# Performance work log

Hardware: AMD Instinct MI355X
Metric: run time of the kernel (lower is better)

## Reference

```python
import jax, jax.numpy as jnp
import numpy as np

L = 8      # subsequence_len
A = 4      # alphabet_size
D = 256    # sketch_dim
SEQ = 16384


def setup_inputs() -> dict:
    key = jax.random.key(0)
    k1, k2, k3 = jax.random.split(key, 3)
    sequence = jax.random.randint(k1, (SEQ,), 0, A)
    # stacked nn.Embedding weights: (L, A, D), init N(0, 0.5)
    hash_emb = 0.5 * jax.random.normal(k2, (L, A, D), dtype=jnp.float32)
    sign_logits = 0.5 * jax.random.normal(k3, (L, A), dtype=jnp.float32)
    return {"sequence": sequence, "hash_emb": hash_emb, "sign_logits": sign_logits}


def _forward(sequence, hash_emb, sign_logits):
    # roll_idx[j, s] = (j - s) % D  so that gather reproduces torch.roll(t, s)[j] = t[(j - s) % D]
    roll_idx = (jnp.arange(D)[:, None] - jnp.arange(D)[None, :]) % D
    p_arr = jnp.arange(1, L + 1, dtype=jnp.float32)           # p = 1..L
    Tp0 = jnp.zeros((L + 1, D), dtype=jnp.float32).at[0, 0].set(1.0)
    Tm0 = jnp.zeros((L + 1, D), dtype=jnp.float32)

    def step(carry, xs):
        Tp, Tm = carry                                         # (L+1, D) each
        c, i = xs
        valid = (c >= 0) & (c < A)
        c_safe = jnp.clip(c, 0, A - 1)
        # eval-mode soft hash: softmax over the embedding row (per level p)
        probs = jax.nn.softmax(hash_emb[:, c_safe, :], axis=-1)   # (L, D)
        sign = jax.nn.sigmoid(sign_logits[:, c_safe])             # (L,)
        denom = (i + 1).astype(jnp.float32)
        # z = p/(i+1); levels with p > i+1 (and invalid chars) are frozen (z=0)
        z = jnp.where((p_arr <= denom) & valid, p_arr / denom, 0.0)  # (L,)
        Tp_prev, Tm_prev = Tp[:L], Tm[:L]                         # (L, D)
        # expected circular shift: out[l, j] = sum_s probs[l, s] * T_prev[l, (j-s)%D]
        stp = jnp.einsum('ljs,ls->lj', Tp_prev[:, roll_idx], probs)
        stm = jnp.einsum('ljs,ls->lj', Tm_prev[:, roll_idx], probs)
        s = sign[:, None]
        upd_p = s * stp + (1.0 - s) * stm
        upd_m = s * stm + (1.0 - s) * stp
        zc = z[:, None]
        new_Tp = Tp.at[1:].set((1.0 - zc) * Tp[1:] + zc * upd_p)
        new_Tm = Tm.at[1:].set((1.0 - zc) * Tm[1:] + zc * upd_m)
        return (new_Tp, new_Tm), None

    step = jax.checkpoint(step)
    (Tp, Tm), _ = jax.lax.scan(step, (Tp0, Tm0), (sequence, jnp.arange(SEQ)))
    return Tp[L] - Tm[L]


def reference(sequence, hash_emb, sign_logits):
    return _forward(sequence, hash_emb, sign_logits)
```

## Files before the change

kernel.cpp:

```cpp
#include <hip/hip_runtime.h>
#include <math.h>

#define LL 8
#define AA 4
#define DD 256
#define KF 129
#define KH 128
#define CLEN 64
#define NES 36
#define LPAD 37

typedef float v2f __attribute__((ext_vector_type(2)));

#define SIX(l2,l1) ((((l2)*((l2)-1))>>1) + (l1))
#define SLOT(s)    ((s)*LPAD + ((s)>>1))

#define V_OFF   0
#define CNT_OFF (2 * KF)

__device__ __forceinline__ float invCN8() {
  constexpr double c = (16384.0 * 16383.0 * 16382.0 * 16381.0 *
                        16380.0 * 16379.0 * 16378.0 * 16377.0) / 40320.0;
  return (float)(1.0 / c);
}

__device__ __forceinline__ v2f cfma(const v2f b, const v2f a, v2f acc) {
  const v2f bb = (v2f){ b.x,  b.x};
  const v2f bw = (v2f){-b.y,  b.y};
  const v2f as = (v2f){ a.y,  a.x};
  acc = __builtin_elementwise_fma(bb, a,  acc);
  acc = __builtin_elementwise_fma(bw, as, acc);
  return acc;
}

template <unsigned MASK>
__device__ __forceinline__ void prodCols(const v2f* __restrict__ A, const v2f* __restrict__ B,
                                         v2f (&o)[NES]) {
#pragma unroll
  for (int l1 = 0; l1 < 8; ++l1) {
    if ((MASK >> l1) & 1) {
#pragma unroll
      for (int l2 = l1 + 1; l2 <= 8; ++l2) {
        v2f acc = A[SIX(l2, l1)] + B[SIX(l2, l1)];
#pragma unroll
        for (int m = l1 + 1; m < l2; ++m) acc = cfma(B[SIX(l2, m)], A[SIX(m, l1)], acc);
        o[SIX(l2, l1)] = acc;
      }
    }
  }
}

template <unsigned MASK>
__device__ __forceinline__ void writeCols(v2f* __restrict__ D, const v2f (&o)[NES]) {
#pragma unroll
  for (int l1 = 0; l1 < 8; ++l1) {
    if ((MASK >> l1) & 1) {
#pragma unroll
      for (int l2 = l1 + 1; l2 <= 8; ++l2) D[SIX(l2, l1)] = o[SIX(l2, l1)];
    }
  }
}

__device__ __forceinline__ void prodFullRA(const v2f (&A)[NES], const v2f* __restrict__ B,
                                           v2f (&o)[NES]) {
#pragma unroll
  for (int l1 = 0; l1 < 8; ++l1) {
#pragma unroll
    for (int l2 = l1 + 1; l2 <= 8; ++l2) {
      v2f acc = A[SIX(l2, l1)] + B[SIX(l2, l1)];
#pragma unroll
      for (int m = l1 + 1; m < l2; ++m) acc = cfma(B[SIX(l2, m)], A[SIX(m, l1)], acc);
      o[SIX(l2, l1)] = acc;
    }
  }
}

__device__ __forceinline__ void prodR(const float* __restrict__ A, const float* __restrict__ B,
                                      float (&o)[NES]) {
#pragma unroll
  for (int l1 = 0; l1 < 8; ++l1) {
#pragma unroll
    for (int l2 = l1 + 1; l2 <= 8; ++l2) {
      float acc = A[SIX(l2, l1)] + B[SIX(l2, l1)];
#pragma unroll
      for (int m = l1 + 1; m < l2; ++m) acc = fmaf(B[SIX(l2, m)], A[SIX(m, l1)], acc);
      o[SIX(l2, l1)] = acc;
    }
  }
}

__global__ __launch_bounds__(256, 1) void kmain(const int* __restrict__ seq,
                                                const float* __restrict__ hemb,
                                                const float* __restrict__ slog,
                                                float* __restrict__ v,
                                                int* __restrict__ cnt,
                                                float* __restrict__ outp) {
  const int blk = blockIdx.x;
  const int t   = threadIdx.x;
  __shared__ __align__(16) float ldsf[9600];
  __shared__ __align__(16) float4 qtab[LL * AA];
  __shared__ float2 twd[256];
  __shared__ float dvr[KF], dvi[KF];
  __shared__ int isLast;

  {
    float sn, cs;
    __sincosf((float)t * 0.0245436926061702596754894014319f, &sn, &cs);
    twd[t] = make_float2(cs, sn);
  }
  __syncthreads();

  {
    const int r  = t >> 3;
    const int g8 = t & 7;
    float4 hv[8];
#pragma unroll
    for (int u = 0; u < 8; ++u)
      hv[u] = *(const float4*)(hemb + r * DD + u * 32 + g8 * 4);
    float mx = -1e30f;
#pragma unroll
    for (int u = 0; u < 8; ++u) {
      mx = fmaxf(mx, fmaxf(fmaxf(hv[u].x, hv[u].y), fmaxf(hv[u].z, hv[u].w)));
    }
    mx = fmaxf(mx, __shfl_xor(mx, 1));
    mx = fmaxf(mx, __shfl_xor(mx, 2));
    mx = fmaxf(mx, __shfl_xor(mx, 4));

    float sum = 0.0f, cr = 0.0f, ci = 0.0f;
    if (blk < KH) {
      const int k = blk;
#pragma unroll
      for (int u = 0; u < 8; ++u) {
        const float ev[4] = {expf(hv[u].x - mx), expf(hv[u].y - mx),
                             expf(hv[u].z - mx), expf(hv[u].w - mx)};
#pragma unroll
        for (int w = 0; w < 4; ++w) {
          const int j = u * 32 + g8 * 4 + w;
          const int m = (j * k) & 255;
          const float2 tv = twd[m];
          sum += ev[w];
          cr = fmaf(ev[w], tv.x, cr);
          ci = fmaf(-ev[w], tv.y, ci);
        }
      }
    } else {
#pragma unroll
      for (int u = 0; u < 8; ++u) {
        const float ev[4] = {expf(hv[u].x - mx), expf(hv[u].y - mx),
                             expf(hv[u].z - mx), expf(hv[u].w - mx)};
        sum += ev[0] + ev[1] + ev[2] + ev[3];
        cr  += (ev[0] - ev[1]) + (ev[2] - ev[3]);
      }
    }
    sum += __shfl_xor(sum, 1); cr += __shfl_xor(cr, 1); ci += __shfl_xor(ci, 1);
    sum += __shfl_xor(sum, 2); cr += __shfl_xor(cr, 2); ci += __shfl_xor(ci, 2);
    sum += __shfl_xor(sum, 4); cr += __shfl_xor(cr, 4); ci += __shfl_xor(ci, 4);

    if (g8 == 0) {
      const float sl = slog[r];
      const float sg = 1.0f / (1.0f + expf(-sl));
      const float q  = fmaf(2.0f, sg, -1.0f);
      const float sc = q / sum;
      const float qr = cr * sc;
      const float qi = ci * sc;
      qtab[r] = make_float4(qr, qr, -qi, qi);
    }
  }
  __syncthreads();

  if (blk < KH) {
    const int k = blk;

    v2f G[NES];
#pragma unroll
    for (int e = 0; e < NES; ++e) G[e] = (v2f){0.f, 0.f};

    const int4* sp = (const int4*)(seq + t * CLEN);
    for (int sb = 0; sb < CLEN / 4; ++sb) {
      const int4 cs = sp[sb];
      const int csy[4] = {cs.x, cs.y, cs.z, cs.w};
#pragma unroll
      for (int u = 0; u < 4; ++u) {
        const int c = csy[u];
        float4 qv[LL];
#pragma unroll
        for (int l = 0; l < LL; ++l) qv[l] = qtab[(l << 2) | c];
#pragma unroll
        for (int l = LL; l >= 1; --l) {
          const float4 q4 = qv[l - 1];
          const v2f qa = (v2f){q4.x, q4.y};
          const v2f qb = (v2f){q4.z, q4.w};
          {
            v2f g = G[SIX(l, l - 1)];
            g.x += q4.x; g.y += q4.w;
            G[SIX(l, l - 1)] = g;
          }
#pragma unroll
          for (int l1 = 0; l1 < l - 1; ++l1) {
            const v2f H  = G[SIX(l - 1, l1)];
            const v2f Hs = (v2f){H.y, H.x};
            v2f g = G[SIX(l, l1)];
            g = __builtin_elementwise_fma(qa, H,  g);
            g = __builtin_elementwise_fma(qb, Hs, g);
            G[SIX(l, l1)] = g;
          }
        }
      }
    }

    v2f* L = (v2f*)ldsf;
    if (t & 1) {
      v2f* D = L + SLOT(t >> 1);
#pragma unroll
      for (int e = 0; e < NES; ++e) D[e] = G[e];
    }
    __syncthreads();
    if (!(t & 1)) {
      v2f o[NES];
      prodFullRA(G, L + SLOT(t >> 1), o);
      v2f* D = L + SLOT(t >> 1);
#pragma unroll
      for (int e = 0; e < NES; ++e) D[e] = o[e];
    }
    __syncthreads();

    const int w = t >> 6;
    const int j = t & 63;
    v2f pc[NES];
    for (int n = 64; n >= 8; n >>= 1) {
      const bool act = (j < n);
      if (act) {
        const v2f* Ab = L + SLOT(2 * j);
        const v2f* Bb = L + SLOT(2 * j + 1);
        switch (w) {
          case 0:  prodCols<0x01>(Ab, Bb, pc); break;
          case 1:  prodCols<0x42>(Ab, Bb, pc); break;
          case 2:  prodCols<0x14>(Ab, Bb, pc); break;
          default: prodCols<0xA8>(Ab, Bb, pc); break;
        }
      }
      __syncthreads();
      if (act) {
        v2f* Db = L + SLOT(j);
        switch (w) {
          case 0:  writeCols<0x01>(Db, pc); break;
          case 1:  writeCols<0x42>(Db, pc); break;
          case 2:  writeCols<0x14>(Db, pc); break;
          default: writeCols<0xA8>(Db, pc); break;
        }
      }
      __syncthreads();
    }

    if (t < 64) {
      v2f sv[LL + 1];
      sv[0] = (v2f){1.f, 0.f};
#pragma unroll
      for (int l = 1; l <= LL; ++l) sv[l] = (v2f){0.f, 0.f};
      for (int gg = 0; gg < 8; ++gg) {
        v2f nv = (v2f){0.f, 0.f};
        if (t >= 1 && t <= LL) {
          nv = sv[t];
          const v2f* Bb = L + SLOT(gg);
          const int rb = (t * (t - 1)) >> 1;
#pragma unroll
          for (int l1 = 0; l1 < 8; ++l1) {
            if (l1 < t) nv = cfma(Bb[rb + l1], sv[l1], nv);
          }
        }
#pragma unroll
        for (int l = 1; l <= LL; ++l) {
          sv[l].x = __shfl(nv.x, l);
          sv[l].y = __shfl(nv.y, l);
        }
      }
      if (t == 0) {
        __hip_atomic_store(&v[2 * k],     sv[LL].x, __ATOMIC_RELEASE, __HIP_MEMORY_SCOPE_AGENT);
        __hip_atomic_store(&v[2 * k + 1], sv[LL].y, __ATOMIC_RELEASE, __HIP_MEMORY_SCOPE_AGENT);
      }
    }
  } else {
    float* Lr = ldsf;
    float Q8[LL][AA];
#pragma unroll
    for (int lc = 0; lc < LL * AA; ++lc) Q8[lc >> 2][lc & 3] = qtab[lc].x;

    float Gr[NES];
#pragma unroll
    for (int e = 0; e < NES; ++e) Gr[e] = 0.f;

    const int4* sp = (const int4*)(seq + t * CLEN);
    for (int sb = 0; sb < CLEN / 4; ++sb) {
      const int4 cs = sp[sb];
      const int csy[4] = {cs.x, cs.y, cs.z, cs.w};
#pragma unroll
      for (int u = 0; u < 4; ++u) {
        const int c = csy[u];
        float Qs[LL];
#pragma unroll
        for (int l = 0; l < LL; ++l) {
          const float qa = (c & 1) ? Q8[l][1] : Q8[l][0];
          const float qb = (c & 1) ? Q8[l][3] : Q8[l][2];
          Qs[l] = (c & 2) ? qb : qa;
        }
#pragma unroll
        for (int l = LL; l >= 1; --l) {
          Gr[SIX(l, l - 1)] += Qs[l - 1];
#pragma unroll
          for (int l1 = 0; l1 < l - 1; ++l1)
            Gr[SIX(l, l1)] = fmaf(Qs[l - 1], Gr[SIX(l - 1, l1)], Gr[SIX(l, l1)]);
        }
      }
    }
#pragma unroll
    for (int e = 0; e < NES; ++e) Lr[t * LPAD + e] = Gr[e];
    __syncthreads();

    float po[NES];
    for (int n = 128; n >= 1; n >>= 1) {
      const bool act = (t < n);
      if (act) prodR(Lr + (2 * t) * LPAD, Lr + (2 * t + 1) * LPAD, po);
      __syncthreads();
      if (act) { for (int e = 0; e < NES; ++e) Lr[t * LPAD + e] = po[e]; }
      __syncthreads();
    }
    if (t == 0) {
      __hip_atomic_store(&v[2 * KH],     Lr[SIX(LL, 0)], __ATOMIC_RELEASE, __HIP_MEMORY_SCOPE_AGENT);
      __hip_atomic_store(&v[2 * KH + 1], 0.0f,           __ATOMIC_RELEASE, __HIP_MEMORY_SCOPE_AGENT);
    }
  }

  __syncthreads();
  if (t == 0) {
    const int old = __hip_atomic_fetch_add(&cnt[0], 1, __ATOMIC_ACQ_REL, __HIP_MEMORY_SCOPE_AGENT);
    isLast = (old == KH) ? 1 : 0;
  }
  __syncthreads();
  if (isLast) {
    if (t < KF) {
      dvr[t] = __hip_atomic_load(&v[2 * t],     __ATOMIC_ACQUIRE, __HIP_MEMORY_SCOPE_AGENT);
      dvi[t] = __hip_atomic_load(&v[2 * t + 1], __ATOMIC_ACQUIRE, __HIP_MEMORY_SCOPE_AGENT);
    }
    if (t == 0) {
      __hip_atomic_store(&cnt[0], 0, __ATOMIC_RELEASE, __HIP_MEMORY_SCOPE_AGENT);
    }
    __syncthreads();
    const float sc = (1.0f / 256.0f) * invCN8();
    float sum = dvr[0] + ((t & 1) ? -dvr[KH] : dvr[KH]);
    for (int k2 = 1; k2 < KH; ++k2) {
      const int m = (t * k2) & 255;
      const float2 wv = twd[m];
      sum = fmaf(2.0f * dvr[k2], wv.x, sum);
      sum = fmaf(-2.0f * dvi[k2], wv.y, sum);
    }
    outp[t] = sum * sc;
  }
}

extern "C" void kernel_launch(void* const* d_in, const int* in_sizes, int n_in,
                              void* d_out, int out_size, void* d_ws, size_t ws_size,
                              hipStream_t stream) {
  (void)in_sizes; (void)n_in; (void)out_size; (void)ws_size;
  const int*   seq  = (const int*)d_in[0];
  const float* hemb = (const float*)d_in[1];
  const float* slog = (const float*)d_in[2];
  float* ws   = (float*)d_ws;
  float* v    = ws + V_OFF;
  int*   cnt  = (int*)(ws + CNT_OFF);
  float* o    = (float*)d_out;

  hipMemsetAsync(cnt, 0, sizeof(int), stream);
  hipLaunchKernelGGL(kmain, dim3(KF), dim3(256), 0, stream, seq, hemb, slog, v, cnt, o);
}
```

Before: 95.86 us.

## Split each frequency's sequence scan across four blocks and pair real frequencies

The grid grows from 129 blocks to 512. Each frequency is now handled by four blocks, each scanning a quarter of the sequence with 16-character chunks per thread. The two real frequencies (k=0 and k=128) are packed into one block using the two lanes of the v2f. Partial transfer operators are written to global memory, and the last block of each group of four combines them through per-frequency atomic counters. This gives more parallelism on a GPU with many compute units, in exchange for an extra cross-block reduction, more atomics and workspace traffic, and repeated setup work in every block.

```diff
diff --git a/kernel.cpp b/kernel.cpp
--- a/kernel.cpp
+++ b/kernel.cpp
@@ -6,7 +6,7 @@
 #define DD 256
 #define KF 129
 #define KH 128
-#define CLEN 64
+#define CLEN 16
 #define NES 36
 #define LPAD 37
 
@@ -16,7 +16,8 @@
 #define SLOT(s)    ((s)*LPAD + ((s)>>1))
 
 #define V_OFF   0
-#define CNT_OFF (2 * KF)
+#define VP_OFF  (2*KF)
+#define CNT_OFF (VP_OFF + 128*4*NES*2)
 
 __device__ __forceinline__ float invCN8() {
   constexpr double c = (16384.0 * 16383.0 * 16382.0 * 16381.0 *
@@ -24,16 +25,21 @@
   return (float)(1.0 / c);
 }
 
-__device__ __forceinline__ v2f cfma(const v2f b, const v2f a, v2f acc) {
-  const v2f bb = (v2f){ b.x,  b.x};
-  const v2f bw = (v2f){-b.y,  b.y};
-  const v2f as = (v2f){ a.y,  a.x};
-  acc = __builtin_elementwise_fma(bb, a,  acc);
-  acc = __builtin_elementwise_fma(bw, as, acc);
-  return acc;
-}
-
-template <unsigned MASK>
+template <bool R2>
+__device__ __forceinline__ v2f opfma(const v2f b, const v2f a, v2f acc) {
+  if (R2) {
+    return __builtin_elementwise_fma(b, a, acc);
+  } else {
+    const v2f bb = (v2f){ b.x,  b.x};
+    const v2f bw = (v2f){-b.y,  b.y};
+    const v2f as = (v2f){ a.y,  a.x};
+    acc = __builtin_elementwise_fma(bb, a,  acc);
+    acc = __builtin_elementwise_fma(bw, as, acc);
+    return acc;
+  }
+}
+
+template <unsigned MASK, bool R2>
 __device__ __forceinline__ void prodCols(const v2f* __restrict__ A, const v2f* __restrict__ B,
                                          v2f (&o)[NES]) {
 #pragma unroll
@@ -43,7 +49,7 @@
       for (int l2 = l1 + 1; l2 <= 8; ++l2) {
         v2f acc = A[SIX(l2, l1)] + B[SIX(l2, l1)];
 #pragma unroll
-        for (int m = l1 + 1; m < l2; ++m) acc = cfma(B[SIX(l2, m)], A[SIX(m, l1)], acc);
+        for (int m = l1 + 1; m < l2; ++m) acc = opfma<R2>(B[SIX(l2, m)], A[SIX(m, l1)], acc);
         o[SIX(l2, l1)] = acc;
       }
     }
@@ -61,6 +67,7 @@
   }
 }
 
+template <bool R2>
 __device__ __forceinline__ void prodFullRA(const v2f (&A)[NES], const v2f* __restrict__ B,
                                            v2f (&o)[NES]) {
 #pragma unroll
@@ -69,132 +76,54 @@
     for (int l2 = l1 + 1; l2 <= 8; ++l2) {
       v2f acc = A[SIX(l2, l1)] + B[SIX(l2, l1)];
 #pragma unroll
-      for (int m = l1 + 1; m < l2; ++m) acc = cfma(B[SIX(l2, m)], A[SIX(m, l1)], acc);
+      for (int m = l1 + 1; m < l2; ++m) acc = opfma<R2>(B[SIX(l2, m)], A[SIX(m, l1)], acc);
       o[SIX(l2, l1)] = acc;
     }
   }
 }
 
-__device__ __forceinline__ void prodR(const float* __restrict__ A, const float* __restrict__ B,
-                                      float (&o)[NES]) {
-#pragma unroll
-  for (int l1 = 0; l1 < 8; ++l1) {
-#pragma unroll
-    for (int l2 = l1 + 1; l2 <= 8; ++l2) {
-      float acc = A[SIX(l2, l1)] + B[SIX(l2, l1)];
-#pragma unroll
-      for (int m = l1 + 1; m < l2; ++m) acc = fmaf(B[SIX(l2, m)], A[SIX(m, l1)], acc);
-      o[SIX(l2, l1)] = acc;
-    }
-  }
-}
-
-__global__ __launch_bounds__(256, 1) void kmain(const int* __restrict__ seq,
-                                                const float* __restrict__ hemb,
-                                                const float* __restrict__ slog,
-                                                float* __restrict__ v,
-                                                int* __restrict__ cnt,
-                                                float* __restrict__ outp) {
-  const int blk = blockIdx.x;
-  const int t   = threadIdx.x;
-  __shared__ __align__(16) float ldsf[9600];
-  __shared__ __align__(16) float4 qtab[LL * AA];
-  __shared__ float2 twd[256];
-  __shared__ float dvr[KF], dvi[KF];
-  __shared__ int isLast;
-
-  {
-    float sn, cs;
-    __sincosf((float)t * 0.0245436926061702596754894014319f, &sn, &cs);
-    twd[t] = make_float2(cs, sn);
-  }
-  __syncthreads();
-
-  {
-    const int r  = t >> 3;
-    const int g8 = t & 7;
-    float4 hv[8];
-#pragma unroll
-    for (int u = 0; u < 8; ++u)
-      hv[u] = *(const float4*)(hemb + r * DD + u * 32 + g8 * 4);
-    float mx = -1e30f;
-#pragma unroll
-    for (int u = 0; u < 8; ++u) {
-      mx = fmaxf(mx, fmaxf(fmaxf(hv[u].x, hv[u].y), fmaxf(hv[u].z, hv[u].w)));
-    }
-    mx = fmaxf(mx, __shfl_xor(mx, 1));
-    mx = fmaxf(mx, __shfl_xor(mx, 2));
-    mx = fmaxf(mx, __shfl_xor(mx, 4));
-
-    float sum = 0.0f, cr = 0.0f, ci = 0.0f;
-    if (blk < KH) {
-      const int k = blk;
-#pragma unroll
-      for (int u = 0; u < 8; ++u) {
-        const float ev[4] = {expf(hv[u].x - mx), expf(hv[u].y - mx),
-                             expf(hv[u].z - mx), expf(hv[u].w - mx)};
-#pragma unroll
-        for (int w = 0; w < 4; ++w) {
-          const int j = u * 32 + g8 * 4 + w;
-          const int m = (j * k) & 255;
-          const float2 tv = twd[m];
-          sum += ev[w];
-          cr = fmaf(ev[w], tv.x, cr);
-          ci = fmaf(-ev[w], tv.y, ci);
-        }
-      }
-    } else {
-#pragma unroll
-      for (int u = 0; u < 8; ++u) {
-        const float ev[4] = {expf(hv[u].x - mx), expf(hv[u].y - mx),
-                             expf(hv[u].z - mx), expf(hv[u].w - mx)};
-        sum += ev[0] + ev[1] + ev[2] + ev[3];
-        cr  += (ev[0] - ev[1]) + (ev[2] - ev[3]);
-      }
-    }
-    sum += __shfl_xor(sum, 1); cr += __shfl_xor(cr, 1); ci += __shfl_xor(ci, 1);
-    sum += __shfl_xor(sum, 2); cr += __shfl_xor(cr, 2); ci += __shfl_xor(ci, 2);
-    sum += __shfl_xor(sum, 4); cr += __shfl_xor(cr, 4); ci += __shfl_xor(ci, 4);
-
-    if (g8 == 0) {
-      const float sl = slog[r];
-      const float sg = 1.0f / (1.0f + expf(-sl));
-      const float q  = fmaf(2.0f, sg, -1.0f);
-      const float sc = q / sum;
-      const float qr = cr * sc;
-      const float qi = ci * sc;
-      qtab[r] = make_float4(qr, qr, -qi, qi);
-    }
-  }
-  __syncthreads();
-
-  if (blk < KH) {
-    const int k = blk;
-
-    v2f G[NES];
-#pragma unroll
-    for (int e = 0; e < NES; ++e) G[e] = (v2f){0.f, 0.f};
-
-    const int4* sp = (const int4*)(seq + t * CLEN);
-    for (int sb = 0; sb < CLEN / 4; ++sb) {
-      const int4 cs = sp[sb];
-      const int csy[4] = {cs.x, cs.y, cs.z, cs.w};
-#pragma unroll
-      for (int u = 0; u < 4; ++u) {
-        const int c = csy[u];
-        float4 qv[LL];
-#pragma unroll
-        for (int l = 0; l < LL; ++l) qv[l] = qtab[(l << 2) | c];
-#pragma unroll
-        for (int l = LL; l >= 1; --l) {
-          const float4 q4 = qv[l - 1];
+template <bool R2>
+__device__ __forceinline__ void applyOp(v2f (&s)[LL + 1], const v2f* __restrict__ op) {
+#pragma unroll
+  for (int l2 = LL; l2 >= 1; --l2) {
+    v2f acc = s[l2];
+#pragma unroll
+    for (int m = 0; m < l2; ++m) acc = opfma<R2>(op[SIX(l2, m)], s[m], acc);
+    s[l2] = acc;
+  }
+}
+
+template <bool R2>
+__device__ __forceinline__ void bodyMain(const int* __restrict__ seq, v2f* L,
+                                         const float4* qtab, int t, int qtr) {
+  v2f G[NES];
+#pragma unroll
+  for (int e = 0; e < NES; ++e) G[e] = (v2f){0.f, 0.f};
+
+  const int ch = qtr * 256 + t;
+  const int4* sp = (const int4*)(seq + ch * CLEN);
+  for (int sb = 0; sb < CLEN / 4; ++sb) {
+    const int4 cs = sp[sb];
+    const int csy[4] = {cs.x, cs.y, cs.z, cs.w};
+#pragma unroll
+    for (int u = 0; u < 4; ++u) {
+      const int c = csy[u];
+      float4 qv[LL];
+#pragma unroll
+      for (int l = 0; l < LL; ++l) qv[l] = qtab[(l << 2) | c];
+#pragma unroll
+      for (int l = LL; l >= 1; --l) {
+        const float4 q4 = qv[l - 1];
+        if (R2) {
+          const v2f qa = (v2f){q4.x, q4.y};
+          G[SIX(l, l - 1)] += qa;
+#pragma unroll
+          for (int l1 = 0; l1 < l - 1; ++l1)
+            G[SIX(l, l1)] = __builtin_elementwise_fma(qa, G[SIX(l - 1, l1)], G[SIX(l, l1)]);
+        } else {
           const v2f qa = (v2f){q4.x, q4.y};
           const v2f qb = (v2f){q4.z, q4.w};
-          {
-            v2f g = G[SIX(l, l - 1)];
-            g.x += q4.x; g.y += q4.w;
-            G[SIX(l, l - 1)] = g;
-          }
+          { v2f g = G[SIX(l, l - 1)]; g.x += q4.x; g.y += q4.w; G[SIX(l, l - 1)] = g; }
 #pragma unroll
           for (int l1 = 0; l1 < l - 1; ++l1) {
             const v2f H  = G[SIX(l - 1, l1)];
@@ -207,133 +136,185 @@
         }
       }
     }
-
-    v2f* L = (v2f*)ldsf;
-    if (t & 1) {
-      v2f* D = L + SLOT(t >> 1);
-#pragma unroll
-      for (int e = 0; e < NES; ++e) D[e] = G[e];
+  }
+
+  if (t & 1) {
+    v2f* D = L + SLOT(t >> 1);
+#pragma unroll
+    for (int e = 0; e < NES; ++e) D[e] = G[e];
+  }
+  __syncthreads();
+  if (!(t & 1)) {
+    v2f o[NES];
+    prodFullRA<R2>(G, L + SLOT(t >> 1), o);
+    v2f* D = L + SLOT(t >> 1);
+#pragma unroll
+    for (int e = 0; e < NES; ++e) D[e] = o[e];
+  }
+  __syncthreads();
+
+  const int w = t >> 6;
+  const int j = t & 63;
+  v2f pc[NES];
+  for (int n = 64; n >= 1; n >>= 1) {
+    const bool act = (j < n);
+    if (act) {
+      const v2f* Ab = L + SLOT(2 * j);
+      const v2f* Bb = L + SLOT(2 * j + 1);
+      switch (w) {
+        case 0:  prodCols<0x01, R2>(Ab, Bb, pc); break;
+        case 1:  prodCols<0x42, R2>(Ab, Bb, pc); break;
+        case 2:  prodCols<0x14, R2>(Ab, Bb, pc); break;
+        default: prodCols<0xA8, R2>(Ab, Bb, pc); break;
+      }
     }
     __syncthreads();
-    if (!(t & 1)) {
-      v2f o[NES];
-      prodFullRA(G, L + SLOT(t >> 1), o);
-      v2f* D = L + SLOT(t >> 1);
-#pragma unroll
-      for (int e = 0; e < NES; ++e) D[e] = o[e];
+    if (act) {
+      v2f* Db = L + SLOT(j);
+      switch (w) {
+        case 0:  writeCols<0x01>(Db, pc); break;
+        case 1:  writeCols<0x42>(Db, pc); break;
+        case 2:  writeCols<0x14>(Db, pc); break;
+        default: writeCols<0xA8>(Db, pc); break;
+      }
     }
     __syncthreads();
-
-    const int w = t >> 6;
-    const int j = t & 63;
-    v2f pc[NES];
-    for (int n = 64; n >= 8; n >>= 1) {
-      const bool act = (j < n);
-      if (act) {
-        const v2f* Ab = L + SLOT(2 * j);
-        const v2f* Bb = L + SLOT(2 * j + 1);
-        switch (w) {
-          case 0:  prodCols<0x01>(Ab, Bb, pc); break;
-          case 1:  prodCols<0x42>(Ab, Bb, pc); break;
-          case 2:  prodCols<0x14>(Ab, Bb, pc); break;
-          default: prodCols<0xA8>(Ab, Bb, pc); break;
+  }
+}
+
+__global__ __launch_bounds__(256) void kmain(const int* __restrict__ seq,
+                                             const float* __restrict__ hemb,
+                                             const float* __restrict__ slog,
+                                             float* __restrict__ v,
+                                             float* __restrict__ vpart,
+                                             int* __restrict__ cnt,
+                                             float* __restrict__ outp) {
+  const int blk = blockIdx.x;
+  const int k   = blk >> 2;
+  const int qtr = blk & 3;
+  const int t   = threadIdx.x;
+  __shared__ __align__(16) float ldsf[9600];
+  __shared__ __align__(16) float4 qtab[LL * AA];
+  __shared__ float2 twd[256];
+  __shared__ float dvr[KF], dvi[KF];
+  __shared__ int isLast, isPairLast;
+
+  {
+    float sn, cs;
+    __sincosf((float)t * 0.0245436926061702596754894014319f, &sn, &cs);
+    twd[t] = make_float2(cs, sn);
+  }
+  __syncthreads();
+
+  {
+    const int r  = t >> 3;
+    const int g8 = t & 7;
+    float4 hv[8];
+#pragma unroll
+    for (int u = 0; u < 8; ++u)
+      hv[u] = *(const float4*)(hemb + r * DD + u * 32 + g8 * 4);
+    float mx = -1e30f;
+#pragma unroll
+    for (int u = 0; u < 8; ++u)
+      mx = fmaxf(mx, fmaxf(fmaxf(hv[u].x, hv[u].y), fmaxf(hv[u].z, hv[u].w)));
+    mx = fmaxf(mx, __shfl_xor(mx, 1));
+    mx = fmaxf(mx, __shfl_xor(mx, 2));
+    mx = fmaxf(mx, __shfl_xor(mx, 4));
+
+    float sum = 0.f, cr = 0.f, ci = 0.f;
+    if (k > 0) {
+#pragma unroll
+      for (int u = 0; u < 8; ++u) {
+        const float ev[4] = {expf(hv[u].x - mx), expf(hv[u].y - mx),
+                             expf(hv[u].z - mx), expf(hv[u].w - mx)};
+#pragma unroll
+        for (int w2 = 0; w2 < 4; ++w2) {
+          const int jj = u * 32 + g8 * 4 + w2;
+          const int m = (jj * k) & 255;
+          const float2 tv = twd[m];
+          sum += ev[w2];
+          cr = fmaf(ev[w2], tv.x, cr);
+          ci = fmaf(-ev[w2], tv.y, ci);
         }
       }
-      __syncthreads();
-      if (act) {
-        v2f* Db = L + SLOT(j);
-        switch (w) {
-          case 0:  writeCols<0x01>(Db, pc); break;
-          case 1:  writeCols<0x42>(Db, pc); break;
-          case 2:  writeCols<0x14>(Db, pc); break;
-          default: writeCols<0xA8>(Db, pc); break;
-        }
-      }
-      __syncthreads();
-    }
-
-    if (t < 64) {
-      v2f sv[LL + 1];
-      sv[0] = (v2f){1.f, 0.f};
-#pragma unroll
-      for (int l = 1; l <= LL; ++l) sv[l] = (v2f){0.f, 0.f};
-      for (int gg = 0; gg < 8; ++gg) {
-        v2f nv = (v2f){0.f, 0.f};
-        if (t >= 1 && t <= LL) {
-          nv = sv[t];
-          const v2f* Bb = L + SLOT(gg);
-          const int rb = (t * (t - 1)) >> 1;
-#pragma unroll
-          for (int l1 = 0; l1 < 8; ++l1) {
-            if (l1 < t) nv = cfma(Bb[rb + l1], sv[l1], nv);
-          }
-        }
-#pragma unroll
-        for (int l = 1; l <= LL; ++l) {
-          sv[l].x = __shfl(nv.x, l);
-          sv[l].y = __shfl(nv.y, l);
-        }
-      }
-      if (t == 0) {
-        __hip_atomic_store(&v[2 * k],     sv[LL].x, __ATOMIC_RELEASE, __HIP_MEMORY_SCOPE_AGENT);
-        __hip_atomic_store(&v[2 * k + 1], sv[LL].y, __ATOMIC_RELEASE, __HIP_MEMORY_SCOPE_AGENT);
-      }
-    }
-  } else {
-    float* Lr = ldsf;
-    float Q8[LL][AA];
-#pragma unroll
-    for (int lc = 0; lc < LL * AA; ++lc) Q8[lc >> 2][lc & 3] = qtab[lc].x;
-
-    float Gr[NES];
-#pragma unroll
-    for (int e = 0; e < NES; ++e) Gr[e] = 0.f;
-
-    const int4* sp = (const int4*)(seq + t * CLEN);
-    for (int sb = 0; sb < CLEN / 4; ++sb) {
-      const int4 cs = sp[sb];
-      const int csy[4] = {cs.x, cs.y, cs.z, cs.w};
-#pragma unroll
-      for (int u = 0; u < 4; ++u) {
-        const int c = csy[u];
-        float Qs[LL];
-#pragma unroll
-        for (int l = 0; l < LL; ++l) {
-          const float qa = (c & 1) ? Q8[l][1] : Q8[l][0];
-          const float qb = (c & 1) ? Q8[l][3] : Q8[l][2];
-          Qs[l] = (c & 2) ? qb : qa;
-        }
-#pragma unroll
-        for (int l = LL; l >= 1; --l) {
-          Gr[SIX(l, l - 1)] += Qs[l - 1];
-#pragma unroll
-          for (int l1 = 0; l1 < l - 1; ++l1)
-            Gr[SIX(l, l1)] = fmaf(Qs[l - 1], Gr[SIX(l - 1, l1)], Gr[SIX(l, l1)]);
-        }
-      }
-    }
-#pragma unroll
-    for (int e = 0; e < NES; ++e) Lr[t * LPAD + e] = Gr[e];
+    } else {
+#pragma unroll
+      for (int u = 0; u < 8; ++u) {
+        const float ev[4] = {expf(hv[u].x - mx), expf(hv[u].y - mx),
+                             expf(hv[u].z - mx), expf(hv[u].w - mx)};
+        sum += ev[0] + ev[1] + ev[2] + ev[3];
+        cr  += (ev[0] - ev[1]) + (ev[2] - ev[3]);
+      }
+    }
+    sum += __shfl_xor(sum, 1); cr += __shfl_xor(cr, 1); ci += __shfl_xor(ci, 1);
+    sum += __shfl_xor(sum, 2); cr += __shfl_xor(cr, 2); ci += __shfl_xor(ci, 2);
+    sum += __shfl_xor(sum, 4); cr += __shfl_xor(cr, 4); ci += __shfl_xor(ci, 4);
+
+    if (g8 == 0) {
+      const float sl = slog[r];
+      const float sg = 1.0f / (1.0f + expf(-sl));
+      const float q  = fmaf(2.0f, sg, -1.0f);
+      if (k > 0) {
+        const float qr = cr * q / sum;
+        const float qi = ci * q / sum;
+        qtab[r] = make_float4(qr, qr, -qi, qi);
+      } else {
+        qtab[r] = make_float4(q, cr * q / sum, 0.f, 0.f);
+      }
+    }
+  }
+  __syncthreads();
+
+  v2f* L = (v2f*)ldsf;
+  if (k == 0) bodyMain<true>(seq, L, qtab, t, qtr);
+  else        bodyMain<false>(seq, L, qtab, t, qtr);
+
+  if (t < NES) {
+    union { v2f v2; double d; } u;
+    u.v2 = L[t];
+    __hip_atomic_store((double*)vpart + (size_t)(k * 4 + qtr) * NES + t, u.d,
+                       __ATOMIC_RELEASE, __HIP_MEMORY_SCOPE_AGENT);
+  }
+  __syncthreads();
+  if (t == 0) {
+    const int old = __hip_atomic_fetch_add(&cnt[1 + k], 1, __ATOMIC_ACQ_REL, __HIP_MEMORY_SCOPE_AGENT);
+    isPairLast = (old == 3) ? 1 : 0;
+  }
+  __syncthreads();
+  if (isPairLast) {
+    if (t < 4 * NES) {
+      union { v2f v2; double d; } u;
+      u.d = __hip_atomic_load((const double*)vpart + (size_t)(k * 4) * NES + t,
+                              __ATOMIC_ACQUIRE, __HIP_MEMORY_SCOPE_AGENT);
+      L[t] = u.v2;
+    }
     __syncthreads();
-
-    float po[NES];
-    for (int n = 128; n >= 1; n >>= 1) {
-      const bool act = (t < n);
-      if (act) prodR(Lr + (2 * t) * LPAD, Lr + (2 * t + 1) * LPAD, po);
-      __syncthreads();
-      if (act) { for (int e = 0; e < NES; ++e) Lr[t * LPAD + e] = po[e]; }
-      __syncthreads();
-    }
     if (t == 0) {
-      __hip_atomic_store(&v[2 * KH],     Lr[SIX(LL, 0)], __ATOMIC_RELEASE, __HIP_MEMORY_SCOPE_AGENT);
-      __hip_atomic_store(&v[2 * KH + 1], 0.0f,           __ATOMIC_RELEASE, __HIP_MEMORY_SCOPE_AGENT);
+      v2f s[LL + 1];
+      s[0] = (k == 0) ? (v2f){1.f, 1.f} : (v2f){1.f, 0.f};
+#pragma unroll
+      for (int l = 1; l <= LL; ++l) s[l] = (v2f){0.f, 0.f};
+      for (int qq = 0; qq < 4; ++qq) {
+        const v2f* op = L + qq * NES;
+        if (k == 0) applyOp<true>(s, op); else applyOp<false>(s, op);
+      }
+      if (k == 0) {
+        __hip_atomic_store(&v[0],          s[LL].x, __ATOMIC_RELEASE, __HIP_MEMORY_SCOPE_AGENT);
+        __hip_atomic_store(&v[1],          0.0f,    __ATOMIC_RELEASE, __HIP_MEMORY_SCOPE_AGENT);
+        __hip_atomic_store(&v[2 * KH],     s[LL].y, __ATOMIC_RELEASE, __HIP_MEMORY_SCOPE_AGENT);
+        __hip_atomic_store(&v[2 * KH + 1], 0.0f,    __ATOMIC_RELEASE, __HIP_MEMORY_SCOPE_AGENT);
+      } else {
+        __hip_atomic_store(&v[2 * k],     s[LL].x, __ATOMIC_RELEASE, __HIP_MEMORY_SCOPE_AGENT);
+        __hip_atomic_store(&v[2 * k + 1], s[LL].y, __ATOMIC_RELEASE, __HIP_MEMORY_SCOPE_AGENT);
+      }
+      __hip_atomic_store(&cnt[1 + k], 0, __ATOMIC_RELAXED, __HIP_MEMORY_SCOPE_AGENT);
     }
   }
 
   __syncthreads();
   if (t == 0) {
     const int old = __hip_atomic_fetch_add(&cnt[0], 1, __ATOMIC_ACQ_REL, __HIP_MEMORY_SCOPE_AGENT);
-    isLast = (old == KH) ? 1 : 0;
+    isLast = (old == 511) ? 1 : 0;
   }
   __syncthreads();
   if (isLast) {
@@ -341,9 +322,8 @@
       dvr[t] = __hip_atomic_load(&v[2 * t],     __ATOMIC_ACQUIRE, __HIP_MEMORY_SCOPE_AGENT);
       dvi[t] = __hip_atomic_load(&v[2 * t + 1], __ATOMIC_ACQUIRE, __HIP_MEMORY_SCOPE_AGENT);
     }
-    if (t == 0) {
+    if (t == 0)
       __hip_atomic_store(&cnt[0], 0, __ATOMIC_RELEASE, __HIP_MEMORY_SCOPE_AGENT);
-    }
     __syncthreads();
     const float sc = (1.0f / 256.0f) * invCN8();
     float sum = dvr[0] + ((t & 1) ? -dvr[KH] : dvr[KH]);
@@ -364,11 +344,12 @@
   const int*   seq  = (const int*)d_in[0];
   const float* hemb = (const float*)d_in[1];
   const float* slog = (const float*)d_in[2];
-  float* ws   = (float*)d_ws;
-  float* v    = ws + V_OFF;
-  int*   cnt  = (int*)(ws + CNT_OFF);
-  float* o    = (float*)d_out;
-
-  hipMemsetAsync(cnt, 0, sizeof(int), stream);
-  hipLaunchKernelGGL(kmain, dim3(KF), dim3(256), 0, stream, seq, hemb, slog, v, cnt, o);
-}
+  float* ws    = (float*)d_ws;
+  float* v     = ws + V_OFF;
+  float* vpart = ws + VP_OFF;
+  int*   cnt   = (int*)(ws + CNT_OFF);
+  float* o     = (float*)d_out;
+
+  hipMemsetAsync(cnt, 0, (1 + KH) * sizeof(int), stream);
+  hipLaunchKernelGGL(kmain, dim3(512), dim3(256), 0, stream, seq, hemb, slog, v, vpart, cnt, o);
+}
```

Result: slower. 114.3 us (+19.3%).

## Double threads per block and halve per-thread chunk length

Applied to the files above, without the earlier changes.

Raises the block size from 256 to 512 threads and halves the sequence chunk each thread scans, so each thread does half the serial recurrence work. The softmax/DFT setup, the tree reductions and the LDS buffer are resized to match, which adds one more reduction level and doubles shared memory. The risk is higher register pressure at 512 threads per block and more synchronisation steps in the reduction.

```diff
diff --git a/kernel.cpp b/kernel.cpp
--- a/kernel.cpp
+++ b/kernel.cpp
@@ -6,7 +6,8 @@
 #define DD 256
 #define KF 129
 #define KH 128
-#define CLEN 64
+#define THR 512
+#define CLEN 32
 #define NES 36
 #define LPAD 37
 
@@ -89,7 +90,7 @@
   }
 }
 
-__global__ __launch_bounds__(256, 1) void kmain(const int* __restrict__ seq,
+__global__ __launch_bounds__(THR, 1) void kmain(const int* __restrict__ seq,
                                                 const float* __restrict__ hemb,
                                                 const float* __restrict__ slog,
                                                 float* __restrict__ v,
@@ -97,13 +98,13 @@
                                                 float* __restrict__ outp) {
   const int blk = blockIdx.x;
   const int t   = threadIdx.x;
-  __shared__ __align__(16) float ldsf[9600];
+  __shared__ __align__(16) float ldsf[19200];
   __shared__ __align__(16) float4 qtab[LL * AA];
   __shared__ float2 twd[256];
   __shared__ float dvr[KF], dvi[KF];
   __shared__ int isLast;
 
-  {
+  if (t < 256) {
     float sn, cs;
     __sincosf((float)t * 0.0245436926061702596754894014319f, &sn, &cs);
     twd[t] = make_float2(cs, sn);
@@ -111,41 +112,41 @@
   __syncthreads();
 
   {
-    const int r  = t >> 3;
-    const int g8 = t & 7;
-    float4 hv[8];
-#pragma unroll
-    for (int u = 0; u < 8; ++u)
-      hv[u] = *(const float4*)(hemb + r * DD + u * 32 + g8 * 4);
+    const int r   = t >> 4;
+    const int g16 = t & 15;
+    float4 hv[4];
+#pragma unroll
+    for (int u = 0; u < 4; ++u)
+      hv[u] = *(const float4*)(hemb + r * DD + u * 64 + g16 * 4);
     float mx = -1e30f;
 #pragma unroll
-    for (int u = 0; u < 8; ++u) {
+    for (int u = 0; u < 4; ++u)
       mx = fmaxf(mx, fmaxf(fmaxf(hv[u].x, hv[u].y), fmaxf(hv[u].z, hv[u].w)));
-    }
     mx = fmaxf(mx, __shfl_xor(mx, 1));
     mx = fmaxf(mx, __shfl_xor(mx, 2));
     mx = fmaxf(mx, __shfl_xor(mx, 4));
-
-    float sum = 0.0f, cr = 0.0f, ci = 0.0f;
+    mx = fmaxf(mx, __shfl_xor(mx, 8));
+
+    float sum = 0.f, cr = 0.f, ci = 0.f;
     if (blk < KH) {
       const int k = blk;
 #pragma unroll
-      for (int u = 0; u < 8; ++u) {
+      for (int u = 0; u < 4; ++u) {
         const float ev[4] = {expf(hv[u].x - mx), expf(hv[u].y - mx),
                              expf(hv[u].z - mx), expf(hv[u].w - mx)};
 #pragma unroll
-        for (int w = 0; w < 4; ++w) {
-          const int j = u * 32 + g8 * 4 + w;
-          const int m = (j * k) & 255;
+        for (int w2 = 0; w2 < 4; ++w2) {
+          const int jj = u * 64 + g16 * 4 + w2;
+          const int m = (jj * k) & 255;
           const float2 tv = twd[m];
-          sum += ev[w];
-          cr = fmaf(ev[w], tv.x, cr);
-          ci = fmaf(-ev[w], tv.y, ci);
+          sum += ev[w2];
+          cr = fmaf(ev[w2], tv.x, cr);
+          ci = fmaf(-ev[w2], tv.y, ci);
         }
       }
     } else {
 #pragma unroll
-      for (int u = 0; u < 8; ++u) {
+      for (int u = 0; u < 4; ++u) {
         const float ev[4] = {expf(hv[u].x - mx), expf(hv[u].y - mx),
                              expf(hv[u].z - mx), expf(hv[u].w - mx)};
         sum += ev[0] + ev[1] + ev[2] + ev[3];
@@ -155,8 +156,9 @@
     sum += __shfl_xor(sum, 1); cr += __shfl_xor(cr, 1); ci += __shfl_xor(ci, 1);
     sum += __shfl_xor(sum, 2); cr += __shfl_xor(cr, 2); ci += __shfl_xor(ci, 2);
     sum += __shfl_xor(sum, 4); cr += __shfl_xor(cr, 4); ci += __shfl_xor(ci, 4);
-
-    if (g8 == 0) {
+    sum += __shfl_xor(sum, 8); cr += __shfl_xor(cr, 8); ci += __shfl_xor(ci, 8);
+
+    if (g16 == 0) {
       const float sl = slog[r];
       const float sg = 1.0f / (1.0f + expf(-sl));
       const float q  = fmaf(2.0f, sg, -1.0f);
@@ -224,10 +226,10 @@
     }
     __syncthreads();
 
-    const int w = t >> 6;
-    const int j = t & 63;
+    const int w = t >> 7;
+    const int j = t & 127;
     v2f pc[NES];
-    for (int n = 64; n >= 8; n >>= 1) {
+    for (int n = 128; n >= 8; n >>= 1) {
       const bool act = (j < n);
       if (act) {
         const v2f* Ab = L + SLOT(2 * j);
@@ -317,7 +319,7 @@
     __syncthreads();
 
     float po[NES];
-    for (int n = 128; n >= 1; n >>= 1) {
+    for (int n = 256; n >= 1; n >>= 1) {
       const bool act = (t < n);
       if (act) prodR(Lr + (2 * t) * LPAD, Lr + (2 * t + 1) * LPAD, po);
       __syncthreads();
@@ -345,15 +347,17 @@
       __hip_atomic_store(&cnt[0], 0, __ATOMIC_RELEASE, __HIP_MEMORY_SCOPE_AGENT);
     }
     __syncthreads();
-    const float sc = (1.0f / 256.0f) * invCN8();
-    float sum = dvr[0] + ((t & 1) ? -dvr[KH] : dvr[KH]);
-    for (int k2 = 1; k2 < KH; ++k2) {
-      const int m = (t * k2) & 255;
-      const float2 wv = twd[m];
-      sum = fmaf(2.0f * dvr[k2], wv.x, sum);
-      sum = fmaf(-2.0f * dvi[k2], wv.y, sum);
-    }
-    outp[t] = sum * sc;
+    if (t < 256) {
+      const float sc = (1.0f / 256.0f) * invCN8();
+      float sum = dvr[0] + ((t & 1) ? -dvr[KH] : dvr[KH]);
+      for (int k2 = 1; k2 < KH; ++k2) {
+        const int m = (t * k2) & 255;
+        const float2 wv = twd[m];
+        sum = fmaf(2.0f * dvr[k2], wv.x, sum);
+        sum = fmaf(-2.0f * dvi[k2], wv.y, sum);
+      }
+      outp[t] = sum * sc;
+    }
   }
 }
 
@@ -370,5 +374,5 @@
   float* o    = (float*)d_out;
 
   hipMemsetAsync(cnt, 0, sizeof(int), stream);
-  hipLaunchKernelGGL(kmain, dim3(KF), dim3(256), 0, stream, seq, hemb, slog, v, cnt, o);
-}
+  hipLaunchKernelGGL(kmain, dim3(KF), dim3(THR), 0, stream, seq, hemb, slog, v, cnt, o);
+}
```

New measurement: 96.38 us. No clear change (+0.5%).
